# Optimization experiments

Measured on AMD Instinct MI355X. Metric: run time of the kernel, lower is better.

Reference implementation:

```python
import jax, jax.numpy as jnp
import numpy as np

N = 50000      # query points
N0 = 50000     # support points
M = 32         # neighbors per query
K = 15         # kernel points
DIM = 3
D_IN = 64
D_OUT = 64
POINT_INFLUENCE = 1.0
KERNEL_RADIUS = 1.5 * POINT_INFLUENCE  # _INFLUENCE_TO_RADIUS * point_influence


def setup_inputs() -> dict:
    key = jax.random.key(0)
    k1, k2, k3, k4, k5 = jax.random.split(key, 5)
    query_points = jax.random.normal(k1, (N, DIM), jnp.float32)
    support_points = jax.random.normal(k2, (N0, DIM), jnp.float32)
    neighbors = jax.random.randint(k3, (N, M), 0, N0 + 1)  # index N0 = shadow point
    x = jax.random.normal(k4, (N0, D_IN), jnp.float32)
    # Kernel point dispositions: fixed center point, rest spread within kernel radius
    # (stand-in for kernel_point_optimization_debug; K_points is a frozen parameter).
    rng = np.random.RandomState(0)
    kp = rng.uniform(-1.0, 1.0, (K, DIM))
    kp[0, :] = 0.0
    kp = kp * (KERNEL_RADIUS / np.max(np.linalg.norm(kp, axis=1)))
    K_points = jnp.asarray(kp, dtype=jnp.float32)
    # Xavier-normal conv weights [K, D_IN, D_OUT]
    std = (2.0 / (D_IN + D_OUT)) ** 0.5
    weight = jax.random.normal(k5, (K, D_IN, D_OUT), jnp.float32) * std
    return {
        "query_points": query_points,
        "support_points": support_points,
        "neighbors": neighbors,
        "x": x,
        "K_points": K_points,
        "weight": weight,
    }


def reference(query_points, support_points, neighbors, x, K_points, weight):
    # Shadow support point far away + zero shadow feature row
    shadow = jnp.full((1, query_points.shape[1]), 1e6, dtype=support_points.dtype)
    sp = jnp.concatenate([support_points, shadow], axis=0)            # [N0+1, 3]
    xp = jnp.concatenate([x, jnp.zeros((1, x.shape[1]), x.dtype)], axis=0)  # [N0+1, d]

    # Gather neighbor coords, center on query point
    neighb_pts = sp[neighbors] - query_points[:, None, :]             # [N, M, 3]
    # Squared distances to each kernel point
    diff = neighb_pts[:, :, None, :] - K_points[None, None, :, :]     # [N, M, K, 3]
    sq_distances = jnp.sum(diff * diff, axis=-1)                      # [N, M, K]

    # Linear influence, then transpose to [N, K, M]
    all_weights = jnp.clip(1.0 - jnp.sqrt(sq_distances) / POINT_INFLUENCE, 0.0)
    all_weights = jnp.swapaxes(all_weights, 1, 2)                     # [N, K, M]

    # Gather neighbor features and aggregate per kernel point
    feats = xp[neighbors]                                             # [N, M, d]
    weighted = jnp.einsum("nkm,nmd->nkd", all_weights, feats)        # [N, K, d]
    # Apply per-kernel-point weight matrices and sum over kernel points
    out = jnp.einsum("nkd,kdo->no", weighted, weight)                # [N, out]
    return out
```

## Files before the change

### kernel.cpp

```cpp
#include <hip/hip_runtime.h>

#define NQ 50000
#define NS 50000
#define MNB 32
#define KP 15
#define DF 64
#define WTS 968
#define WQS 40

typedef __bf16 bf16x8 __attribute__((ext_vector_type(8)));
typedef float  f32x4  __attribute__((ext_vector_type(4)));
typedef float  f32x2  __attribute__((ext_vector_type(2)));

__device__ __forceinline__ unsigned short bf1(float f) {
    union { __bf16 h; unsigned short s; } r; r.h = (__bf16)f; return r.s;
}
__device__ __forceinline__ unsigned pk2(float a, float b) {
    union { __bf16 h[2]; unsigned u; } r;
    r.h[0] = (__bf16)a; r.h[1] = (__bf16)b; return r.u;
}

#define PERM_LO 0x05040100u
#define PERM_HI 0x07060302u

__global__ __launch_bounds__(256) void conv_prep(const float* __restrict__ W,
                                                 uint4* __restrict__ wBf,
                                                 const float* __restrict__ x,
                                                 uint4* __restrict__ xBf) {
    const int b = blockIdx.x;
    if (b < 30) {
        const int chunk = b * 256 + threadIdx.x;
        const int tc = chunk >> 6, c = chunk & 63;
        union { unsigned short s[8]; uint4 u; } pk;
        #pragma unroll
        for (int j = 0; j < 8; ++j)
            pk.s[j] = bf1(W[(size_t)(tc * 8 + j) * 64 + c]);
        wBf[chunk] = pk.u;
    } else {
        const int t = (b - 30) * 256 + threadIdx.x;
        if (t < (NS * DF) / 8) {
            const float4* __restrict__ x4 = (const float4*)x;
            const float4 a = x4[t * 2];
            const float4 c = x4[t * 2 + 1];
            uint4 o;
            o.x = pk2(a.x, a.y); o.y = pk2(a.z, a.w);
            o.z = pk2(c.x, c.y); o.w = pk2(c.z, c.w);
            xBf[t] = o;
        }
    }
}

__global__ __launch_bounds__(1024, 8) void kpconv_fused(
    const float* __restrict__ qp, const float* __restrict__ sp,
    const int* __restrict__ nb, const uint2* __restrict__ xb,
    const float* __restrict__ kpts, const uint4* __restrict__ wBf,
    float* __restrict__ out)
{
    __shared__ struct {
        __align__(16) unsigned short wt[16 * WTS];
        __align__(16) unsigned short wq[16][16 * WQS];
        __align__(16) unsigned int   ids[16][MNB];
    } sm;

    const int tid  = threadIdx.x;
    const int lane = tid & 63;
    const int wv   = __builtin_amdgcn_readfirstlane(tid >> 6);
    const int kh = lane >> 5, m = lane & 31;
    const int n0 = blockIdx.x * 16;
    const int n  = n0 + wv;

    const int id = nb[n * MNB + m];
    const float qx = qp[n * 3 + 0], qy = qp[n * 3 + 1], qz = qp[n * 3 + 2];
    float sx = 1e6f, sy = 1e6f, sz = 1e6f;
    if (id < NS) { sx = sp[id * 3 + 0]; sy = sp[id * 3 + 1]; sz = sp[id * 3 + 2]; }
    const float rx = sx - qx, ry = sy - qy, rz = sz - qz;
    float wk[8], wmax = 0.0f;
    #pragma unroll
    for (int jj = 0; jj < 4; ++jj) {
        const int ka = kh * 8 + jj;
        const int kb0 = ka + 4;
        const int kb = (kb0 < KP) ? kb0 : 0;
        const f32x2 dx = (f32x2){rx, rx} - (f32x2){kpts[ka*3+0], kpts[kb*3+0]};
        const f32x2 dy = (f32x2){ry, ry} - (f32x2){kpts[ka*3+1], kpts[kb*3+1]};
        const f32x2 dz = (f32x2){rz, rz} - (f32x2){kpts[ka*3+2], kpts[kb*3+2]};
        const f32x2 d2 = dx * dx + dy * dy + dz * dz;
        const float wa = fmaxf(1.0f - __builtin_amdgcn_sqrtf(d2.x), 0.0f);
        const float wb = fmaxf(1.0f - __builtin_amdgcn_sqrtf(d2.y), 0.0f);
        wk[jj] = wa; wk[jj + 4] = wb;
        wmax = fmaxf(wmax, fmaxf(wa, wb));
    }
    const unsigned long long bal = __ballot(wmax > 0.0f);
    const unsigned comb = (unsigned)(bal & 0xFFFFFFFFull) | (unsigned)(bal >> 32);
    const int A = __popc(comb);
    const bool act = (comb >> m) & 1u;
    const unsigned mlow = (1u << m) - 1u;
    const int p = act ? __popc(comb & mlow) : (A + __popc(~comb & mlow));
    const int s = (p & 3) * 8 + (p >> 2);
    const float gate = act ? 1.0f : 0.0f;
    #pragma unroll
    for (int jj = 0; jj < 8; ++jj)
        sm.wq[wv][(kh * 8 + jj) * WQS + s] = bf1(wk[jj] * gate);
    if (kh == 0) sm.ids[wv][p] = act ? (unsigned)id : 0u;

    const int cl = lane & 15, q = lane >> 4;
    union { uint4 u; bf16x8 v; } af;
    af.u = *(const uint4*)&sm.wq[wv][cl * WQS + q * 8];
    uint2 r[8];
    #pragma unroll
    for (int j = 0; j < 8; ++j) {
        r[j] = (uint2){0u, 0u};
        if (4 * j < A)
            r[j] = xb[(size_t)sm.ids[wv][4 * j + q] * 16 + cl];
    }
    union { uint4 u; bf16x8 v; } bfr[4];
    #pragma unroll
    for (int pr = 0; pr < 4; ++pr) {
        const uint2 e = r[2 * pr], o = r[2 * pr + 1];
        ((unsigned*)&bfr[0].u)[pr] = __builtin_amdgcn_perm(o.x, e.x, PERM_LO);
        ((unsigned*)&bfr[1].u)[pr] = __builtin_amdgcn_perm(o.x, e.x, PERM_HI);
        ((unsigned*)&bfr[2].u)[pr] = __builtin_amdgcn_perm(o.y, e.y, PERM_LO);
        ((unsigned*)&bfr[3].u)[pr] = __builtin_amdgcn_perm(o.y, e.y, PERM_HI);
    }
    const f32x4 zero = (f32x4){0.f, 0.f, 0.f, 0.f};
    f32x4 acc1[4];
    #pragma unroll
    for (int cb = 0; cb < 4; ++cb)
        acc1[cb] = __builtin_amdgcn_mfma_f32_16x16x32_bf16(af.v, bfr[cb].v, zero, 0, 0, 0);

    #pragma unroll
    for (int i = 0; i < 4; ++i) {
        const int k = q * 4 + i;
        if (k < KP) {
            uint2 pkd;
            pkd.x = pk2(acc1[0][i], acc1[1][i]);
            pkd.y = pk2(acc1[2][i], acc1[3][i]);
            *(uint2*)&sm.wt[wv * WTS + k * 64 + cl * 4] = pkd;
        }
    }
    __syncthreads();
    if (wv >= 4) return;

    f32x4 dacc = (f32x4){0.f, 0.f, 0.f, 0.f};
    #pragma unroll 6
    for (int ks = 0; ks < 30; ++ks) {
        const bf16x8 a = *(const bf16x8*)&sm.wt[cl * WTS + ks * 32 + q * 8];
        union { uint4 u; bf16x8 v; } bu;
        bu.u = wBf[(4 * ks + q) * 64 + wv * 16 + cl];
        dacc = __builtin_amdgcn_mfma_f32_16x16x32_bf16(a, bu.v, dacc, 0, 0, 0);
    }
    #pragma unroll
    for (int i = 0; i < 4; ++i)
        out[(size_t)(n0 + q * 4 + i) * 64 + wv * 16 + cl] = dacc[i];
}

extern "C" void kernel_launch(void* const* d_in, const int* in_sizes, int n_in,
                              void* d_out, int out_size, void* d_ws, size_t ws_size,
                              hipStream_t stream) {
    const float* qp   = (const float*)d_in[0];
    const float* sp   = (const float*)d_in[1];
    const int*   nb   = (const int*)d_in[2];
    const float* x    = (const float*)d_in[3];
    const float* kpts = (const float*)d_in[4];
    const float* W    = (const float*)d_in[5];
    float* out = (float*)d_out;

    uint4* wBf = (uint4*)d_ws;
    uint4* xBf = (uint4*)((char*)d_ws + 122880);

    hipLaunchKernelGGL(conv_prep, dim3(30 + (NS * DF / 8 + 255) / 256), dim3(256),
                       0, stream, W, wBf, x, xBf);
    hipLaunchKernelGGL(kpconv_fused, dim3(NQ / 16), dim3(1024), 0, stream,
                       qp, sp, nb, (const uint2*)xBf, kpts, wBf, out);
}
```

Before: 120.7 us.

## Make fused KPConv kernel persistent with prefetch and double-buffered shared tile

Turns the fused kernel into a persistent grid of 512 blocks that loop over 16-query tiles. Each iteration prefetches the next tile's neighbor indices, query coords and support coords, and alternates between two shared-memory buffers so only one barrier is needed per tile. Further changes: XOR-swizzled influence matrix layout to cut LDS bank conflicts, 16-bit neighbor ids read as one vector, a weight layout regrouped per output wave for contiguous loads, and two independent MFMA accumulators in the second GEMM. The cost is fewer resident blocks and idle waves 4-15 during the second GEMM, so latency hiding across waves is reduced.

```diff
diff --git a/kernel.cpp b/kernel.cpp
--- a/kernel.cpp
+++ b/kernel.cpp
@@ -5,8 +5,10 @@
 #define MNB 32
 #define KP 15
 #define DF 64
+#define NT 3125
+#define GRID 512
 #define WTS 968
-#define WQS 40
+#define WQR 32
 
 typedef __bf16 bf16x8 __attribute__((ext_vector_type(8)));
 typedef float  f32x4  __attribute__((ext_vector_type(4)));
@@ -35,7 +37,8 @@
         #pragma unroll
         for (int j = 0; j < 8; ++j)
             pk.s[j] = bf1(W[(size_t)(tc * 8 + j) * 64 + c]);
-        wBf[chunk] = pk.u;
+        const int ks = tc >> 2, qq = tc & 3, wvv = c >> 4, cll = c & 15;
+        wBf[(wvv * 30 + ks) * 64 + qq * 16 + cll] = pk.u;
     } else {
         const int t = (b - 30) * 256 + threadIdx.x;
         if (t < (NS * DF) / 8) {
@@ -57,100 +60,140 @@
     float* __restrict__ out)
 {
     __shared__ struct {
-        __align__(16) unsigned short wt[16 * WTS];
-        __align__(16) unsigned short wq[16][16 * WQS];
-        __align__(16) unsigned int   ids[16][MNB];
+        __align__(16) unsigned short wt[2][16 * WTS];
+        __align__(16) unsigned short wq[16][16 * WQR];
+        __align__(16) unsigned short ids[16][MNB];
     } sm;
 
     const int tid  = threadIdx.x;
     const int lane = tid & 63;
     const int wv   = __builtin_amdgcn_readfirstlane(tid >> 6);
     const int kh = lane >> 5, m = lane & 31;
-    const int n0 = blockIdx.x * 16;
-    const int n  = n0 + wv;
-
-    const int id = nb[n * MNB + m];
-    const float qx = qp[n * 3 + 0], qy = qp[n * 3 + 1], qz = qp[n * 3 + 2];
-    float sx = 1e6f, sy = 1e6f, sz = 1e6f;
-    if (id < NS) { sx = sp[id * 3 + 0]; sy = sp[id * 3 + 1]; sz = sp[id * 3 + 2]; }
-    const float rx = sx - qx, ry = sy - qy, rz = sz - qz;
-    float wk[8], wmax = 0.0f;
-    #pragma unroll
-    for (int jj = 0; jj < 4; ++jj) {
-        const int ka = kh * 8 + jj;
-        const int kb0 = ka + 4;
-        const int kb = (kb0 < KP) ? kb0 : 0;
-        const f32x2 dx = (f32x2){rx, rx} - (f32x2){kpts[ka*3+0], kpts[kb*3+0]};
-        const f32x2 dy = (f32x2){ry, ry} - (f32x2){kpts[ka*3+1], kpts[kb*3+1]};
-        const f32x2 dz = (f32x2){rz, rz} - (f32x2){kpts[ka*3+2], kpts[kb*3+2]};
-        const f32x2 d2 = dx * dx + dy * dy + dz * dz;
-        const float wa = fmaxf(1.0f - __builtin_amdgcn_sqrtf(d2.x), 0.0f);
-        const float wb = fmaxf(1.0f - __builtin_amdgcn_sqrtf(d2.y), 0.0f);
-        wk[jj] = wa; wk[jj + 4] = wb;
-        wmax = fmaxf(wmax, fmaxf(wa, wb));
+    const int cl = lane & 15, q = lane >> 4;
+
+    int t = blockIdx.x;
+    int id; float qx, qy, qz, sx, sy, sz;
+    {
+        const int n = t * 16 + wv;
+        id = nb[n * MNB + m];
+        qx = qp[n * 3 + 0]; qy = qp[n * 3 + 1]; qz = qp[n * 3 + 2];
+        sx = 1e6f; sy = 1e6f; sz = 1e6f;
+        if (id < NS) { sx = sp[id * 3 + 0]; sy = sp[id * 3 + 1]; sz = sp[id * 3 + 2]; }
     }
-    const unsigned long long bal = __ballot(wmax > 0.0f);
-    const unsigned comb = (unsigned)(bal & 0xFFFFFFFFull) | (unsigned)(bal >> 32);
-    const int A = __popc(comb);
-    const bool act = (comb >> m) & 1u;
-    const unsigned mlow = (1u << m) - 1u;
-    const int p = act ? __popc(comb & mlow) : (A + __popc(~comb & mlow));
-    const int s = (p & 3) * 8 + (p >> 2);
-    const float gate = act ? 1.0f : 0.0f;
-    #pragma unroll
-    for (int jj = 0; jj < 8; ++jj)
-        sm.wq[wv][(kh * 8 + jj) * WQS + s] = bf1(wk[jj] * gate);
-    if (kh == 0) sm.ids[wv][p] = act ? (unsigned)id : 0u;
-
-    const int cl = lane & 15, q = lane >> 4;
-    union { uint4 u; bf16x8 v; } af;
-    af.u = *(const uint4*)&sm.wq[wv][cl * WQS + q * 8];
-    uint2 r[8];
-    #pragma unroll
-    for (int j = 0; j < 8; ++j) {
-        r[j] = (uint2){0u, 0u};
-        if (4 * j < A)
-            r[j] = xb[(size_t)sm.ids[wv][4 * j + q] * 16 + cl];
+
+    int buf = 0;
+    while (t < NT) {
+        const int n0 = t * 16;
+        const int t2 = t + GRID;
+
+        int id2 = NS; float qx2 = 0.f, qy2 = 0.f, qz2 = 0.f;
+        if (t2 < NT) {
+            const int n2 = t2 * 16 + wv;
+            id2 = nb[n2 * MNB + m];
+            qx2 = qp[n2 * 3 + 0]; qy2 = qp[n2 * 3 + 1]; qz2 = qp[n2 * 3 + 2];
+        }
+
+        const float rx = sx - qx, ry = sy - qy, rz = sz - qz;
+        float wk[8], wmax = 0.0f;
+        #pragma unroll
+        for (int jj = 0; jj < 4; ++jj) {
+            const int ka = kh * 8 + jj;
+            const int kb0 = ka + 4;
+            const int kb = (kb0 < KP) ? kb0 : 0;
+            const f32x2 dx = (f32x2){rx, rx} - (f32x2){kpts[ka*3+0], kpts[kb*3+0]};
+            const f32x2 dy = (f32x2){ry, ry} - (f32x2){kpts[ka*3+1], kpts[kb*3+1]};
+            const f32x2 dz = (f32x2){rz, rz} - (f32x2){kpts[ka*3+2], kpts[kb*3+2]};
+            const f32x2 d2 = dx * dx + dy * dy + dz * dz;
+            const float wa = fmaxf(1.0f - __builtin_amdgcn_sqrtf(d2.x), 0.0f);
+            const float wb = fmaxf(1.0f - __builtin_amdgcn_sqrtf(d2.y), 0.0f);
+            wk[jj] = wa; wk[jj + 4] = wb;
+            wmax = fmaxf(wmax, fmaxf(wa, wb));
+        }
+        const unsigned long long bal = __ballot(wmax > 0.0f);
+        const unsigned comb = (unsigned)(bal & 0xFFFFFFFFull) | (unsigned)(bal >> 32);
+        const int A = __popc(comb);
+        const bool act = (comb >> m) & 1u;
+        const unsigned mlow = (1u << m) - 1u;
+        const int p = act ? __popc(comb & mlow) : (A + __popc(~comb & mlow));
+        const int s = (p & 3) * 8 + (p >> 2);
+        const float gate = act ? 1.0f : 0.0f;
+        #pragma unroll
+        for (int jj = 0; jj < 8; ++jj) {
+            const int row = kh * 8 + jj;
+            const int off = row * WQR + ((((s >> 3) ^ (row & 3))) << 3) + (s & 7);
+            sm.wq[wv][off] = bf1(wk[jj] * gate);
+        }
+        if (kh == 0) sm.ids[wv][s] = (unsigned short)(act ? id : 0);
+
+        union { uint4 u; bf16x8 v; } af;
+        af.u = *(const uint4*)&sm.wq[wv][cl * WQR + ((q ^ (cl & 3)) << 3)];
+        union { uint4 u; unsigned short h[8]; } iu;
+        iu.u = *(const uint4*)&sm.ids[wv][q * 8];
+        uint2 r[8];
+        #pragma unroll
+        for (int j = 0; j < 8; ++j) {
+            r[j] = (uint2){0u, 0u};
+            if (4 * j < A)
+                r[j] = xb[(size_t)iu.h[j] * 16 + cl];
+        }
+        union { uint4 u; bf16x8 v; } bfr[4];
+        #pragma unroll
+        for (int pr = 0; pr < 4; ++pr) {
+            const uint2 e = r[2 * pr], o = r[2 * pr + 1];
+            ((unsigned*)&bfr[0].u)[pr] = __builtin_amdgcn_perm(o.x, e.x, PERM_LO);
+            ((unsigned*)&bfr[1].u)[pr] = __builtin_amdgcn_perm(o.x, e.x, PERM_HI);
+            ((unsigned*)&bfr[2].u)[pr] = __builtin_amdgcn_perm(o.y, e.y, PERM_LO);
+            ((unsigned*)&bfr[3].u)[pr] = __builtin_amdgcn_perm(o.y, e.y, PERM_HI);
+        }
+        const f32x4 zero = (f32x4){0.f, 0.f, 0.f, 0.f};
+        f32x4 acc1[4];
+        #pragma unroll
+        for (int cb = 0; cb < 4; ++cb)
+            acc1[cb] = __builtin_amdgcn_mfma_f32_16x16x32_bf16(af.v, bfr[cb].v, zero, 0, 0, 0);
+
+        #pragma unroll
+        for (int i = 0; i < 4; ++i) {
+            const int k = q * 4 + i;
+            if (k < KP) {
+                uint2 pkd;
+                pkd.x = pk2(acc1[0][i], acc1[1][i]);
+                pkd.y = pk2(acc1[2][i], acc1[3][i]);
+                *(uint2*)&sm.wt[buf][wv * WTS + k * 64 + cl * 4] = pkd;
+            }
+        }
+
+        float sx2 = 1e6f, sy2 = 1e6f, sz2 = 1e6f;
+        if (id2 < NS) {
+            sx2 = sp[id2 * 3 + 0]; sy2 = sp[id2 * 3 + 1]; sz2 = sp[id2 * 3 + 2];
+        }
+
+        __syncthreads();
+
+        if (wv < 4) {
+            const unsigned short* wtb = sm.wt[buf];
+            const uint4* wb = wBf + (wv * 30) * 64 + q * 16 + cl;
+            f32x4 d0 = (f32x4){0.f, 0.f, 0.f, 0.f};
+            f32x4 d1 = (f32x4){0.f, 0.f, 0.f, 0.f};
+            #pragma unroll 5
+            for (int ks = 0; ks < 30; ks += 2) {
+                const bf16x8 a0 = *(const bf16x8*)&wtb[cl * WTS + ks * 32 + q * 8];
+                const bf16x8 a1 = *(const bf16x8*)&wtb[cl * WTS + ks * 32 + 32 + q * 8];
+                union { uint4 u; bf16x8 v; } b0, b1;
+                b0.u = wb[ks * 64];
+                b1.u = wb[ks * 64 + 64];
+                d0 = __builtin_amdgcn_mfma_f32_16x16x32_bf16(a0, b0.v, d0, 0, 0, 0);
+                d1 = __builtin_amdgcn_mfma_f32_16x16x32_bf16(a1, b1.v, d1, 0, 0, 0);
+            }
+            const f32x4 dacc = d0 + d1;
+            #pragma unroll
+            for (int i = 0; i < 4; ++i)
+                out[(size_t)(n0 + q * 4 + i) * 64 + wv * 16 + cl] = dacc[i];
+        }
+
+        buf ^= 1;
+        t = t2;
+        id = id2; qx = qx2; qy = qy2; qz = qz2; sx = sx2; sy = sy2; sz = sz2;
     }
-    union { uint4 u; bf16x8 v; } bfr[4];
-    #pragma unroll
-    for (int pr = 0; pr < 4; ++pr) {
-        const uint2 e = r[2 * pr], o = r[2 * pr + 1];
-        ((unsigned*)&bfr[0].u)[pr] = __builtin_amdgcn_perm(o.x, e.x, PERM_LO);
-        ((unsigned*)&bfr[1].u)[pr] = __builtin_amdgcn_perm(o.x, e.x, PERM_HI);
-        ((unsigned*)&bfr[2].u)[pr] = __builtin_amdgcn_perm(o.y, e.y, PERM_LO);
-        ((unsigned*)&bfr[3].u)[pr] = __builtin_amdgcn_perm(o.y, e.y, PERM_HI);
-    }
-    const f32x4 zero = (f32x4){0.f, 0.f, 0.f, 0.f};
-    f32x4 acc1[4];
-    #pragma unroll
-    for (int cb = 0; cb < 4; ++cb)
-        acc1[cb] = __builtin_amdgcn_mfma_f32_16x16x32_bf16(af.v, bfr[cb].v, zero, 0, 0, 0);
-
-    #pragma unroll
-    for (int i = 0; i < 4; ++i) {
-        const int k = q * 4 + i;
-        if (k < KP) {
-            uint2 pkd;
-            pkd.x = pk2(acc1[0][i], acc1[1][i]);
-            pkd.y = pk2(acc1[2][i], acc1[3][i]);
-            *(uint2*)&sm.wt[wv * WTS + k * 64 + cl * 4] = pkd;
-        }
-    }
-    __syncthreads();
-    if (wv >= 4) return;
-
-    f32x4 dacc = (f32x4){0.f, 0.f, 0.f, 0.f};
-    #pragma unroll 6
-    for (int ks = 0; ks < 30; ++ks) {
-        const bf16x8 a = *(const bf16x8*)&sm.wt[cl * WTS + ks * 32 + q * 8];
-        union { uint4 u; bf16x8 v; } bu;
-        bu.u = wBf[(4 * ks + q) * 64 + wv * 16 + cl];
-        dacc = __builtin_amdgcn_mfma_f32_16x16x32_bf16(a, bu.v, dacc, 0, 0, 0);
-    }
-    #pragma unroll
-    for (int i = 0; i < 4; ++i)
-        out[(size_t)(n0 + q * 4 + i) * 64 + wv * 16 + cl] = dacc[i];
 }
 
 extern "C" void kernel_launch(void* const* d_in, const int* in_sizes, int n_in,
@@ -169,6 +212,6 @@
 
     hipLaunchKernelGGL(conv_prep, dim3(30 + (NS * DF / 8 + 255) / 256), dim3(256),
                        0, stream, W, wBf, x, xBf);
-    hipLaunchKernelGGL(kpconv_fused, dim3(NQ / 16), dim3(1024), 0, stream,
+    hipLaunchKernelGGL(kpconv_fused, dim3(GRID), dim3(1024), 0, stream,
                        qp, sp, nb, (const uint2*)xBf, kpts, wBf, out);
 }
```

After: 132.4 us. 1.1x slower.

## Make fused kpconv persistent with producer/consumer warp specialization and double-buffered LDS

Applied to the files above, without the earlier changes.

Replaces the one-tile-per-block launch with a persistent grid of 512 blocks. Each block loops over tiles of 12 queries. Twelve waves produce the per-kernel-point aggregated features into a double-buffered LDS tile, while four waves run the weight GEMM on the previous tile, so gather and GEMM overlap. The weight matrix is re-laid out for contiguous per-wave loads, and neighbor ids are stored as 16-bit values read with one vector load. Only 12 of the 16 MFMA rows do useful work, and every tile iteration pays a block-wide barrier.

```diff
diff --git a/kernel.cpp b/kernel.cpp
--- a/kernel.cpp
+++ b/kernel.cpp
@@ -5,6 +5,9 @@
 #define MNB 32
 #define KP 15
 #define DF 64
+#define NPW 12
+#define NT 4167
+#define GRID 512
 #define WTS 968
 #define WQS 40
 
@@ -35,7 +38,8 @@
         #pragma unroll
         for (int j = 0; j < 8; ++j)
             pk.s[j] = bf1(W[(size_t)(tc * 8 + j) * 64 + c]);
-        wBf[chunk] = pk.u;
+        const int ks = tc >> 2, qq = tc & 3, g = c >> 4, cll = c & 15;
+        wBf[(g * 30 + ks) * 64 + qq * 16 + cll] = pk.u;
     } else {
         const int t = (b - 30) * 256 + threadIdx.x;
         if (t < (NS * DF) / 8) {
@@ -57,100 +61,130 @@
     float* __restrict__ out)
 {
     __shared__ struct {
-        __align__(16) unsigned short wt[16 * WTS];
-        __align__(16) unsigned short wq[16][16 * WQS];
-        __align__(16) unsigned int   ids[16][MNB];
+        __align__(16) unsigned short wt[2][13 * WTS];
+        __align__(16) unsigned short wq[NPW][16 * WQS];
+        __align__(16) unsigned short ids[NPW][MNB];
     } sm;
 
     const int tid  = threadIdx.x;
     const int lane = tid & 63;
     const int wv   = __builtin_amdgcn_readfirstlane(tid >> 6);
     const int kh = lane >> 5, m = lane & 31;
-    const int n0 = blockIdx.x * 16;
-    const int n  = n0 + wv;
-
-    const int id = nb[n * MNB + m];
-    const float qx = qp[n * 3 + 0], qy = qp[n * 3 + 1], qz = qp[n * 3 + 2];
-    float sx = 1e6f, sy = 1e6f, sz = 1e6f;
-    if (id < NS) { sx = sp[id * 3 + 0]; sy = sp[id * 3 + 1]; sz = sp[id * 3 + 2]; }
-    const float rx = sx - qx, ry = sy - qy, rz = sz - qz;
-    float wk[8], wmax = 0.0f;
-    #pragma unroll
-    for (int jj = 0; jj < 4; ++jj) {
-        const int ka = kh * 8 + jj;
-        const int kb0 = ka + 4;
-        const int kb = (kb0 < KP) ? kb0 : 0;
-        const f32x2 dx = (f32x2){rx, rx} - (f32x2){kpts[ka*3+0], kpts[kb*3+0]};
-        const f32x2 dy = (f32x2){ry, ry} - (f32x2){kpts[ka*3+1], kpts[kb*3+1]};
-        const f32x2 dz = (f32x2){rz, rz} - (f32x2){kpts[ka*3+2], kpts[kb*3+2]};
-        const f32x2 d2 = dx * dx + dy * dy + dz * dz;
-        const float wa = fmaxf(1.0f - __builtin_amdgcn_sqrtf(d2.x), 0.0f);
-        const float wb = fmaxf(1.0f - __builtin_amdgcn_sqrtf(d2.y), 0.0f);
-        wk[jj] = wa; wk[jj + 4] = wb;
-        wmax = fmaxf(wmax, fmaxf(wa, wb));
+    const int cl = lane & 15, q = lane >> 4;
+
+    if (tid < 121) {
+        ((uint4*)&sm.wt[0][12 * WTS])[tid] = (uint4){0u, 0u, 0u, 0u};
+        ((uint4*)&sm.wt[1][12 * WTS])[tid] = (uint4){0u, 0u, 0u, 0u};
     }
-    const unsigned long long bal = __ballot(wmax > 0.0f);
-    const unsigned comb = (unsigned)(bal & 0xFFFFFFFFull) | (unsigned)(bal >> 32);
-    const int A = __popc(comb);
-    const bool act = (comb >> m) & 1u;
-    const unsigned mlow = (1u << m) - 1u;
-    const int p = act ? __popc(comb & mlow) : (A + __popc(~comb & mlow));
-    const int s = (p & 3) * 8 + (p >> 2);
-    const float gate = act ? 1.0f : 0.0f;
-    #pragma unroll
-    for (int jj = 0; jj < 8; ++jj)
-        sm.wq[wv][(kh * 8 + jj) * WQS + s] = bf1(wk[jj] * gate);
-    if (kh == 0) sm.ids[wv][p] = act ? (unsigned)id : 0u;
-
-    const int cl = lane & 15, q = lane >> 4;
-    union { uint4 u; bf16x8 v; } af;
-    af.u = *(const uint4*)&sm.wq[wv][cl * WQS + q * 8];
-    uint2 r[8];
-    #pragma unroll
-    for (int j = 0; j < 8; ++j) {
-        r[j] = (uint2){0u, 0u};
-        if (4 * j < A)
-            r[j] = xb[(size_t)sm.ids[wv][4 * j + q] * 16 + cl];
+
+    int buf = 0;
+    for (int t = blockIdx.x; t < NT + GRID; t += GRID) {
+        if (wv < NPW) {
+            const int n = t * NPW + wv;
+            if (t < NT && n < NQ) {
+                const int id = nb[n * MNB + m];
+                const float qx = qp[n * 3 + 0], qy = qp[n * 3 + 1], qz = qp[n * 3 + 2];
+                float sx = 1e6f, sy = 1e6f, sz = 1e6f;
+                if (id < NS) { sx = sp[id * 3 + 0]; sy = sp[id * 3 + 1]; sz = sp[id * 3 + 2]; }
+                const float rx = sx - qx, ry = sy - qy, rz = sz - qz;
+                float wk[8], wmax = 0.0f;
+                #pragma unroll
+                for (int jj = 0; jj < 4; ++jj) {
+                    const int ka = kh * 8 + jj;
+                    const int kb0 = ka + 4;
+                    const int kb = (kb0 < KP) ? kb0 : 0;
+                    const f32x2 dx = (f32x2){rx, rx} - (f32x2){kpts[ka*3+0], kpts[kb*3+0]};
+                    const f32x2 dy = (f32x2){ry, ry} - (f32x2){kpts[ka*3+1], kpts[kb*3+1]};
+                    const f32x2 dz = (f32x2){rz, rz} - (f32x2){kpts[ka*3+2], kpts[kb*3+2]};
+                    const f32x2 d2 = dx * dx + dy * dy + dz * dz;
+                    const float wa = fmaxf(1.0f - __builtin_amdgcn_sqrtf(d2.x), 0.0f);
+                    const float wb = fmaxf(1.0f - __builtin_amdgcn_sqrtf(d2.y), 0.0f);
+                    wk[jj] = wa; wk[jj + 4] = wb;
+                    wmax = fmaxf(wmax, fmaxf(wa, wb));
+                }
+                const unsigned long long bal = __ballot(wmax > 0.0f);
+                const unsigned comb = (unsigned)(bal & 0xFFFFFFFFull) | (unsigned)(bal >> 32);
+                const int A = __popc(comb);
+                const bool act = (comb >> m) & 1u;
+                const unsigned mlow = (1u << m) - 1u;
+                const int p = act ? __popc(comb & mlow) : (A + __popc(~comb & mlow));
+                const int s = (p & 3) * 8 + (p >> 2);
+                const float gate = act ? 1.0f : 0.0f;
+                #pragma unroll
+                for (int jj = 0; jj < 8; ++jj)
+                    sm.wq[wv][(kh * 8 + jj) * WQS + s] = bf1(wk[jj] * gate);
+                if (kh == 0) sm.ids[wv][s] = (unsigned short)(act ? id : 0);
+
+                union { uint4 u; bf16x8 v; } af;
+                af.u = *(const uint4*)&sm.wq[wv][cl * WQS + q * 8];
+                union { uint4 u; unsigned short h[8]; } iu;
+                iu.u = *(const uint4*)&sm.ids[wv][q * 8];
+                uint2 r[8];
+                #pragma unroll
+                for (int j = 0; j < 8; ++j) {
+                    r[j] = (uint2){0u, 0u};
+                    if (4 * j < A)
+                        r[j] = xb[(size_t)iu.h[j] * 16 + cl];
+                }
+                union { uint4 u; bf16x8 v; } bfr[4];
+                #pragma unroll
+                for (int pr = 0; pr < 4; ++pr) {
+                    const uint2 e = r[2 * pr], o = r[2 * pr + 1];
+                    ((unsigned*)&bfr[0].u)[pr] = __builtin_amdgcn_perm(o.x, e.x, PERM_LO);
+                    ((unsigned*)&bfr[1].u)[pr] = __builtin_amdgcn_perm(o.x, e.x, PERM_HI);
+                    ((unsigned*)&bfr[2].u)[pr] = __builtin_amdgcn_perm(o.y, e.y, PERM_LO);
+                    ((unsigned*)&bfr[3].u)[pr] = __builtin_amdgcn_perm(o.y, e.y, PERM_HI);
+                }
+                const f32x4 zero = (f32x4){0.f, 0.f, 0.f, 0.f};
+                f32x4 acc1[4];
+                #pragma unroll
+                for (int cb = 0; cb < 4; ++cb)
+                    acc1[cb] = __builtin_amdgcn_mfma_f32_16x16x32_bf16(af.v, bfr[cb].v, zero, 0, 0, 0);
+
+                #pragma unroll
+                for (int i = 0; i < 4; ++i) {
+                    const int k = q * 4 + i;
+                    if (k < KP) {
+                        uint2 pkd;
+                        pkd.x = pk2(acc1[0][i], acc1[1][i]);
+                        pkd.y = pk2(acc1[2][i], acc1[3][i]);
+                        *(uint2*)&sm.wt[buf][wv * WTS + k * 64 + cl * 4] = pkd;
+                    }
+                }
+            }
+        } else if (t > (int)blockIdx.x) {
+            const int tp = t - GRID;
+            const int n0 = tp * NPW;
+            const int g  = wv - NPW;
+            const unsigned short* wtb = sm.wt[buf ^ 1];
+            const int arow = (cl < NPW) ? cl : NPW;
+            const uint4* wb = wBf + (g * 30) * 64 + q * 16 + cl;
+            f32x4 d0 = (f32x4){0.f, 0.f, 0.f, 0.f};
+            f32x4 d1 = (f32x4){0.f, 0.f, 0.f, 0.f};
+            __builtin_amdgcn_s_setprio(1);
+            #pragma unroll 5
+            for (int ks = 0; ks < 30; ks += 2) {
+                const bf16x8 a0 = *(const bf16x8*)&wtb[arow * WTS + ks * 32 + q * 8];
+                const bf16x8 a1 = *(const bf16x8*)&wtb[arow * WTS + (ks + 1) * 32 + q * 8];
+                union { uint4 u; bf16x8 v; } b0, b1;
+                b0.u = wb[ks * 64];
+                b1.u = wb[(ks + 1) * 64];
+                d0 = __builtin_amdgcn_mfma_f32_16x16x32_bf16(a0, b0.v, d0, 0, 0, 0);
+                d1 = __builtin_amdgcn_mfma_f32_16x16x32_bf16(a1, b1.v, d1, 0, 0, 0);
+            }
+            __builtin_amdgcn_s_setprio(0);
+            const f32x4 dacc = d0 + d1;
+            #pragma unroll
+            for (int i = 0; i < 4; ++i) {
+                const int rrow = q * 4 + i;
+                const int n = n0 + rrow;
+                if (rrow < NPW && n < NQ)
+                    out[(size_t)n * 64 + g * 16 + cl] = dacc[i];
+            }
+        }
+        __syncthreads();
+        buf ^= 1;
     }
-    union { uint4 u; bf16x8 v; } bfr[4];
-    #pragma unroll
-    for (int pr = 0; pr < 4; ++pr) {
-        const uint2 e = r[2 * pr], o = r[2 * pr + 1];
-        ((unsigned*)&bfr[0].u)[pr] = __builtin_amdgcn_perm(o.x, e.x, PERM_LO);
-        ((unsigned*)&bfr[1].u)[pr] = __builtin_amdgcn_perm(o.x, e.x, PERM_HI);
-        ((unsigned*)&bfr[2].u)[pr] = __builtin_amdgcn_perm(o.y, e.y, PERM_LO);
-        ((unsigned*)&bfr[3].u)[pr] = __builtin_amdgcn_perm(o.y, e.y, PERM_HI);
-    }
-    const f32x4 zero = (f32x4){0.f, 0.f, 0.f, 0.f};
-    f32x4 acc1[4];
-    #pragma unroll
-    for (int cb = 0; cb < 4; ++cb)
-        acc1[cb] = __builtin_amdgcn_mfma_f32_16x16x32_bf16(af.v, bfr[cb].v, zero, 0, 0, 0);
-
-    #pragma unroll
-    for (int i = 0; i < 4; ++i) {
-        const int k = q * 4 + i;
-        if (k < KP) {
-            uint2 pkd;
-            pkd.x = pk2(acc1[0][i], acc1[1][i]);
-            pkd.y = pk2(acc1[2][i], acc1[3][i]);
-            *(uint2*)&sm.wt[wv * WTS + k * 64 + cl * 4] = pkd;
-        }
-    }
-    __syncthreads();
-    if (wv >= 4) return;
-
-    f32x4 dacc = (f32x4){0.f, 0.f, 0.f, 0.f};
-    #pragma unroll 6
-    for (int ks = 0; ks < 30; ++ks) {
-        const bf16x8 a = *(const bf16x8*)&sm.wt[cl * WTS + ks * 32 + q * 8];
-        union { uint4 u; bf16x8 v; } bu;
-        bu.u = wBf[(4 * ks + q) * 64 + wv * 16 + cl];
-        dacc = __builtin_amdgcn_mfma_f32_16x16x32_bf16(a, bu.v, dacc, 0, 0, 0);
-    }
-    #pragma unroll
-    for (int i = 0; i < 4; ++i)
-        out[(size_t)(n0 + q * 4 + i) * 64 + wv * 16 + cl] = dacc[i];
 }
 
 extern "C" void kernel_launch(void* const* d_in, const int* in_sizes, int n_in,
@@ -169,6 +203,6 @@
 
     hipLaunchKernelGGL(conv_prep, dim3(30 + (NS * DF / 8 + 255) / 256), dim3(256),
                        0, stream, W, wBf, x, xBf);
-    hipLaunchKernelGGL(kpconv_fused, dim3(NQ / 16), dim3(1024), 0, stream,
+    hipLaunchKernelGGL(kpconv_fused, dim3(GRID), dim3(1024), 0, stream,
                        qp, sp, nb, (const uint2*)xBf, kpts, wBf, out);
 }
```

New measurement: 123.9 us. 1.03x slower.

## Process 32 queries per block, drop neighbor compaction, use all waves in second GEMM

Applied to the files above, without the earlier changes.

Each block now handles 32 queries instead of 16, with each wave computing two queries. The ballot/popcount compaction of active neighbors is removed: all 32 neighbor features are gathered unconditionally, and the first MFMA is transposed so that kernel-point weights are the B operand. The second GEMM uses all 16 waves, split into row tiles, column tiles and K halves, with a cross-wave shared-memory reduction. It also adds an XOR-swizzled LDS layout and a repacked, zero-padded weight buffer. The aim is to keep all waves busy during the dense stage and to avoid bank conflicts, at the cost of gathering shadow or inactive neighbors instead of skipping them.

```diff
diff --git a/kernel.cpp b/kernel.cpp
--- a/kernel.cpp
+++ b/kernel.cpp
@@ -4,13 +4,11 @@
 #define NS 50000
 #define MNB 32
 #define KP 15
-#define DF 64
-#define WTS 968
-#define WQS 40
+#define QPB 32
+#define NBLK 1563
 
 typedef __bf16 bf16x8 __attribute__((ext_vector_type(8)));
 typedef float  f32x4  __attribute__((ext_vector_type(4)));
-typedef float  f32x2  __attribute__((ext_vector_type(2)));
 
 __device__ __forceinline__ unsigned short bf1(float f) {
     union { __bf16 h; unsigned short s; } r; r.h = (__bf16)f; return r.s;
@@ -28,23 +26,26 @@
                                                  const float* __restrict__ x,
                                                  uint4* __restrict__ xBf) {
     const int b = blockIdx.x;
-    if (b < 30) {
-        const int chunk = b * 256 + threadIdx.x;
-        const int tc = chunk >> 6, c = chunk & 63;
+    if (b < 32) {
+        const int c = b * 256 + threadIdx.x;
+        const int cl = c & 15, qq = (c >> 4) & 3, ks = (c >> 6) & 31, cc = c >> 11;
+        const int k0 = ks * 32 + qq * 8;
+        const int o  = cc * 16 + cl;
         union { unsigned short s[8]; uint4 u; } pk;
         #pragma unroll
         for (int j = 0; j < 8; ++j)
-            pk.s[j] = bf1(W[(size_t)(tc * 8 + j) * 64 + c]);
-        wBf[chunk] = pk.u;
+            pk.s[j] = (k0 + j < KP * 64) ? bf1(W[(size_t)(k0 + j) * 64 + o])
+                                         : (unsigned short)0;
+        wBf[c] = pk.u;
     } else {
-        const int t = (b - 30) * 256 + threadIdx.x;
-        if (t < (NS * DF) / 8) {
+        const int t = (b - 32) * 256 + threadIdx.x;
+        if (t < (NS * 64) / 8) {
             const float4* __restrict__ x4 = (const float4*)x;
             const float4 a = x4[t * 2];
-            const float4 c = x4[t * 2 + 1];
+            const float4 c2 = x4[t * 2 + 1];
             uint4 o;
-            o.x = pk2(a.x, a.y); o.y = pk2(a.z, a.w);
-            o.z = pk2(c.x, c.y); o.w = pk2(c.z, c.w);
+            o.x = pk2(a.x, a.y);  o.y = pk2(a.z, a.w);
+            o.z = pk2(c2.x, c2.y); o.w = pk2(c2.z, c2.w);
             xBf[t] = o;
         }
     }
@@ -57,100 +58,134 @@
     float* __restrict__ out)
 {
     __shared__ struct {
-        __align__(16) unsigned short wt[16 * WTS];
-        __align__(16) unsigned short wq[16][16 * WQS];
-        __align__(16) unsigned int   ids[16][MNB];
+        __align__(16) unsigned short wt[QPB * 1024];
+        union {
+            float4 rc4[QPB][MNB];
+            f32x4  red[8][64];
+        } u;
     } sm;
 
     const int tid  = threadIdx.x;
     const int lane = tid & 63;
     const int wv   = __builtin_amdgcn_readfirstlane(tid >> 6);
-    const int kh = lane >> 5, m = lane & 31;
-    const int n0 = blockIdx.x * 16;
-    const int n  = n0 + wv;
-
-    const int id = nb[n * MNB + m];
-    const float qx = qp[n * 3 + 0], qy = qp[n * 3 + 1], qz = qp[n * 3 + 2];
-    float sx = 1e6f, sy = 1e6f, sz = 1e6f;
-    if (id < NS) { sx = sp[id * 3 + 0]; sy = sp[id * 3 + 1]; sz = sp[id * 3 + 2]; }
-    const float rx = sx - qx, ry = sy - qy, rz = sz - qz;
-    float wk[8], wmax = 0.0f;
-    #pragma unroll
-    for (int jj = 0; jj < 4; ++jj) {
-        const int ka = kh * 8 + jj;
-        const int kb0 = ka + 4;
-        const int kb = (kb0 < KP) ? kb0 : 0;
-        const f32x2 dx = (f32x2){rx, rx} - (f32x2){kpts[ka*3+0], kpts[kb*3+0]};
-        const f32x2 dy = (f32x2){ry, ry} - (f32x2){kpts[ka*3+1], kpts[kb*3+1]};
-        const f32x2 dz = (f32x2){rz, rz} - (f32x2){kpts[ka*3+2], kpts[kb*3+2]};
-        const f32x2 d2 = dx * dx + dy * dy + dz * dz;
-        const float wa = fmaxf(1.0f - __builtin_amdgcn_sqrtf(d2.x), 0.0f);
-        const float wb = fmaxf(1.0f - __builtin_amdgcn_sqrtf(d2.y), 0.0f);
-        wk[jj] = wa; wk[jj + 4] = wb;
-        wmax = fmaxf(wmax, fmaxf(wa, wb));
-    }
-    const unsigned long long bal = __ballot(wmax > 0.0f);
-    const unsigned comb = (unsigned)(bal & 0xFFFFFFFFull) | (unsigned)(bal >> 32);
-    const int A = __popc(comb);
-    const bool act = (comb >> m) & 1u;
-    const unsigned mlow = (1u << m) - 1u;
-    const int p = act ? __popc(comb & mlow) : (A + __popc(~comb & mlow));
-    const int s = (p & 3) * 8 + (p >> 2);
-    const float gate = act ? 1.0f : 0.0f;
-    #pragma unroll
-    for (int jj = 0; jj < 8; ++jj)
-        sm.wq[wv][(kh * 8 + jj) * WQS + s] = bf1(wk[jj] * gate);
-    if (kh == 0) sm.ids[wv][p] = act ? (unsigned)id : 0u;
-
     const int cl = lane & 15, q = lane >> 4;
-    union { uint4 u; bf16x8 v; } af;
-    af.u = *(const uint4*)&sm.wq[wv][cl * WQS + q * 8];
-    uint2 r[8];
+    const int n0 = blockIdx.x * QPB;
+
+    const int   kidx = (cl < KP) ? cl : (KP - 1);
+    const float kx = kpts[kidx * 3 + 0];
+    const float ky = kpts[kidx * 3 + 1];
+    const float kz = kpts[kidx * 3 + 2];
+    const float gate = (cl < KP) ? 1.0f : 0.0f;
+
+    {
+        const int m  = lane & 31, gh = lane >> 5;
+        const int n  = n0 + wv * 2 + gh;
+        float rx = 1e6f, ry = 1e6f, rz = 1e6f; int idc = 0;
+        if (n < NQ) {
+            const int id = nb[n * MNB + m];
+            const float qx = qp[n * 3 + 0], qy = qp[n * 3 + 1], qz = qp[n * 3 + 2];
+            float sx = 1e6f, sy = 1e6f, sz = 1e6f;
+            if (id < NS) { sx = sp[id*3+0]; sy = sp[id*3+1]; sz = sp[id*3+2]; }
+            rx = sx - qx; ry = sy - qy; rz = sz - qz;
+            idc = (id < NS) ? id : 0;
+        }
+        sm.u.rc4[wv * 2 + gh][m] = (float4){rx, ry, rz, __int_as_float(idc)};
+    }
+
+    const int ga = wv * 2, gb = ga + 1;
+
+    float wA[8], wB[8]; unsigned idA[8], idB[8];
     #pragma unroll
     for (int j = 0; j < 8; ++j) {
-        r[j] = (uint2){0u, 0u};
-        if (4 * j < A)
-            r[j] = xb[(size_t)sm.ids[wv][4 * j + q] * 16 + cl];
-    }
-    union { uint4 u; bf16x8 v; } bfr[4];
-    #pragma unroll
-    for (int pr = 0; pr < 4; ++pr) {
-        const uint2 e = r[2 * pr], o = r[2 * pr + 1];
-        ((unsigned*)&bfr[0].u)[pr] = __builtin_amdgcn_perm(o.x, e.x, PERM_LO);
-        ((unsigned*)&bfr[1].u)[pr] = __builtin_amdgcn_perm(o.x, e.x, PERM_HI);
-        ((unsigned*)&bfr[2].u)[pr] = __builtin_amdgcn_perm(o.y, e.y, PERM_LO);
-        ((unsigned*)&bfr[3].u)[pr] = __builtin_amdgcn_perm(o.y, e.y, PERM_HI);
-    }
+        const float4 rc = sm.u.rc4[ga][4 * j + q];
+        const float dx = rc.x - kx, dy = rc.y - ky, dz = rc.z - kz;
+        const float d2 = dx * dx + dy * dy + dz * dz;
+        wA[j]  = fmaxf(1.0f - __builtin_amdgcn_sqrtf(d2), 0.0f) * gate;
+        idA[j] = __float_as_uint(rc.w);
+    }
+    uint2 rA[8];
+    #pragma unroll
+    for (int j = 0; j < 8; ++j) rA[j] = xb[(size_t)idA[j] * 16 + cl];
+    #pragma unroll
+    for (int j = 0; j < 8; ++j) {
+        const float4 rc = sm.u.rc4[gb][4 * j + q];
+        const float dx = rc.x - kx, dy = rc.y - ky, dz = rc.z - kz;
+        const float d2 = dx * dx + dy * dy + dz * dz;
+        wB[j]  = fmaxf(1.0f - __builtin_amdgcn_sqrtf(d2), 0.0f) * gate;
+        idB[j] = __float_as_uint(rc.w);
+    }
+    uint2 rB[8];
+    #pragma unroll
+    for (int j = 0; j < 8; ++j) rB[j] = xb[(size_t)idB[j] * 16 + cl];
+
     const f32x4 zero = (f32x4){0.f, 0.f, 0.f, 0.f};
-    f32x4 acc1[4];
-    #pragma unroll
-    for (int cb = 0; cb < 4; ++cb)
-        acc1[cb] = __builtin_amdgcn_mfma_f32_16x16x32_bf16(af.v, bfr[cb].v, zero, 0, 0, 0);
-
-    #pragma unroll
-    for (int i = 0; i < 4; ++i) {
-        const int k = q * 4 + i;
-        if (k < KP) {
-            uint2 pkd;
-            pkd.x = pk2(acc1[0][i], acc1[1][i]);
-            pkd.y = pk2(acc1[2][i], acc1[3][i]);
-            *(uint2*)&sm.wt[wv * WTS + k * 64 + cl * 4] = pkd;
-        }
-    }
+    #pragma unroll
+    for (int gg = 0; gg < 2; ++gg) {
+        const float*  w  = gg ? wB : wA;
+        const uint2*  r  = gg ? rB : rA;
+        const int     g  = gg ? gb : ga;
+        union { uint4 u; bf16x8 v; } wf;
+        wf.u.x = pk2(w[0], w[1]); wf.u.y = pk2(w[2], w[3]);
+        wf.u.z = pk2(w[4], w[5]); wf.u.w = pk2(w[6], w[7]);
+        union { uint4 u; bf16x8 v; } af[4];
+        #pragma unroll
+        for (int pr = 0; pr < 4; ++pr) {
+            const uint2 e = r[2 * pr], o = r[2 * pr + 1];
+            ((unsigned*)&af[0].u)[pr] = __builtin_amdgcn_perm(o.x, e.x, PERM_LO);
+            ((unsigned*)&af[1].u)[pr] = __builtin_amdgcn_perm(o.x, e.x, PERM_HI);
+            ((unsigned*)&af[2].u)[pr] = __builtin_amdgcn_perm(o.y, e.y, PERM_LO);
+            ((unsigned*)&af[3].u)[pr] = __builtin_amdgcn_perm(o.y, e.y, PERM_HI);
+        }
+        f32x4 acc[4];
+        #pragma unroll
+        for (int cb = 0; cb < 4; ++cb)
+            acc[cb] = __builtin_amdgcn_mfma_f32_16x16x32_bf16(af[cb].v, wf.v, zero, 0, 0, 0);
+        unsigned pkd[8];
+        #pragma unroll
+        for (int i = 0; i < 4; ++i) {
+            pkd[2 * i]     = pk2(acc[0][i], acc[1][i]);
+            pkd[2 * i + 1] = pk2(acc[2][i], acc[3][i]);
+        }
+        const unsigned key = (unsigned)(((g & 7) ^ (cl & 7)) << 4);
+        char* base = (char*)sm.wt + g * 2048;
+        const unsigned i0 = (unsigned)(cl * 128 + q * 32);
+        *(uint4*)(base + ((i0)      ^ key)) = (uint4){pkd[0], pkd[1], pkd[2], pkd[3]};
+        *(uint4*)(base + ((i0 + 16) ^ key)) = (uint4){pkd[4], pkd[5], pkd[6], pkd[7]};
+    }
+
     __syncthreads();
-    if (wv >= 4) return;
-
-    f32x4 dacc = (f32x4){0.f, 0.f, 0.f, 0.f};
-    #pragma unroll 6
-    for (int ks = 0; ks < 30; ++ks) {
-        const bf16x8 a = *(const bf16x8*)&sm.wt[cl * WTS + ks * 32 + q * 8];
-        union { uint4 u; bf16x8 v; } bu;
-        bu.u = wBf[(4 * ks + q) * 64 + wv * 16 + cl];
-        dacc = __builtin_amdgcn_mfma_f32_16x16x32_bf16(a, bu.v, dacc, 0, 0, 0);
-    }
-    #pragma unroll
-    for (int i = 0; i < 4; ++i)
-        out[(size_t)(n0 + q * 4 + i) * 64 + wv * 16 + cl] = dacc[i];
+
+    const int h  = wv >> 3;
+    const int tl = wv & 7;
+    const int rc = tl >> 2, cc = tl & 3;
+    const char* abase = (const char*)sm.wt + (rc * 16 + cl) * 2048;
+    const unsigned akey = (unsigned)((cl & 7) << 4);
+    const uint4* wb = wBf + (((cc * 32 + h * 16) * 4 + q) * 16 + cl);
+    f32x4 d0 = zero, d1 = zero;
+    #pragma unroll 4
+    for (int it = 0; it < 16; it += 2) {
+        const int ks0 = h * 16 + it;
+        const unsigned kk  = (unsigned)((((ks0 >> 1) & 7)) << 4);
+        const unsigned ia0 = (unsigned)(ks0 * 64 + q * 16);
+        const bf16x8 a0 = *(const bf16x8*)(abase + ((ia0)      ^ akey ^ kk));
+        const bf16x8 a1 = *(const bf16x8*)(abase + ((ia0 + 64) ^ akey ^ kk));
+        union { uint4 u; bf16x8 v; } b0, b1;
+        b0.u = wb[it * 64];
+        b1.u = wb[it * 64 + 64];
+        d0 = __builtin_amdgcn_mfma_f32_16x16x32_bf16(a0, b0.v, d0, 0, 0, 0);
+        d1 = __builtin_amdgcn_mfma_f32_16x16x32_bf16(a1, b1.v, d1, 0, 0, 0);
+    }
+    f32x4 dd = d0 + d1;
+    if (h == 1) sm.u.red[tl][lane] = dd;
+    __syncthreads();
+    if (h == 0) {
+        dd += sm.u.red[tl][lane];
+        #pragma unroll
+        for (int i = 0; i < 4; ++i) {
+            const int n = n0 + rc * 16 + q * 4 + i;
+            if (n < NQ) out[(size_t)n * 64 + cc * 16 + cl] = dd[i];
+        }
+    }
 }
 
 extern "C" void kernel_launch(void* const* d_in, const int* in_sizes, int n_in,
@@ -165,10 +200,10 @@
     float* out = (float*)d_out;
 
     uint4* wBf = (uint4*)d_ws;
-    uint4* xBf = (uint4*)((char*)d_ws + 122880);
-
-    hipLaunchKernelGGL(conv_prep, dim3(30 + (NS * DF / 8 + 255) / 256), dim3(256),
+    uint4* xBf = (uint4*)((char*)d_ws + 131072);
+
+    hipLaunchKernelGGL(conv_prep, dim3(32 + (NS * 64 / 8 + 255) / 256), dim3(256),
                        0, stream, W, wBf, x, xBf);
-    hipLaunchKernelGGL(kpconv_fused, dim3(NQ / 16), dim3(1024), 0, stream,
+    hipLaunchKernelGGL(kpconv_fused, dim3(NBLK), dim3(1024), 0, stream,
                        qp, sp, nb, (const uint2*)xBf, kpts, wBf, out);
 }
```

Result: slower. 145.7 us (+20.7%).
